# Kernel optimization log

Measured on AMD Instinct MI355X. Metric: run time of the kernel, lower is better.

The kernel has to match this reference:

```python
import jax, jax.numpy as jnp
import numpy as np

H, DK, DV, D, EPS = 4, 64, 64, 256, 1e-5

def setup_inputs() -> dict:
    key = jax.random.key(0)
    ks = jax.random.split(key, 12)
    B, L = 8, 2048
    s = 0.02
    return {
        "q": jax.random.normal(ks[0], (B, L, D), jnp.float32),
        "k": jax.random.normal(ks[1], (B, L, D), jnp.float32),
        "v": jax.random.normal(ks[2], (B, L, D), jnp.float32),
        "mask": jax.random.randint(ks[3], (B, L), 0, 2) > 0,
        "wq": s * jax.random.normal(ks[4], (D, H * DK), jnp.float32),
        "bq": jnp.zeros((H * DK,), jnp.float32),
        "wk": s * jax.random.normal(ks[5], (D, H * DK), jnp.float32),
        "bk": jnp.zeros((H * DK,), jnp.float32),
        "wv": s * jax.random.normal(ks[6], (D, H * DV), jnp.float32),
        "bv": jnp.zeros((H * DV,), jnp.float32),
        "wf": s * jax.random.normal(ks[7], (H * DV, D), jnp.float32),
        "bf": jnp.zeros((D,), jnp.float32),
        "gamma": jnp.ones((D,), jnp.float32),
        "beta": jnp.zeros((D,), jnp.float32),
    }

def reference(q, k, v, mask, wq, bq, wk, bk, wv, bv, wf, bf, gamma, beta):
    B, Lq, _ = q.shape
    Lk = k.shape[1]
    residual = q
    qh = (q @ wq + bq).reshape(B, Lq, H, DK)  # [B,L,H,dk]
    kh = (k @ wk + bk).reshape(B, Lk, H, DK)
    vh = (v @ wv + bv).reshape(B, Lk, H, DV)
    scores = jnp.einsum("bqhd,bkhd->bhqk", qh, kh) / jnp.sqrt(jnp.float32(DK))
    scores = jnp.where(mask[:, None, None, :], -jnp.inf, scores)
    attn = jax.nn.softmax(scores, axis=-1)  # [B,H,Lq,Lk]
    out = jnp.einsum("bhqk,bkhd->bqhd", attn, vh).reshape(B, Lq, H * DV)
    out = out @ wf + bf  # dropout is identity in eval mode
    x = out + residual
    mu = jnp.mean(x, axis=-1, keepdims=True)
    var = jnp.var(x, axis=-1, keepdims=True)
    out = gamma * (x - mu) * jax.lax.rsqrt(var + EPS) + beta
    # attn reshaped to torch layout (n_head*B, Lq, Lk)
    attn_t = attn.transpose(1, 0, 2, 3).reshape(H * B, Lq, Lk)
    return (out, attn_t)
```

## Files before the change

kernel.cpp:

```cpp
#include <hip/hip_runtime.h>
#include <hip/hip_bf16.h>

#define NH 4
#define DKV 64
#define DM 256
#define NB 8
#define NL 2048
#define LN_EPS 1e-5f

typedef __hip_bfloat16 bf16;
typedef __attribute__((ext_vector_type(8))) short short8;
typedef __attribute__((ext_vector_type(4))) float f32x4;

#define MFMA(a, b, c) __builtin_amdgcn_mfma_f32_16x16x32_bf16((a), (b), (c), 0, 0, 0)

__device__ __forceinline__ short f2bf(float f) {
  __hip_bfloat16 h = __float2bfloat16(f);
  return *reinterpret_cast<short*>(&h);
}

__global__ __launch_bounds__(256) void prep_kernel(
    const float* __restrict__ wq, const float* __restrict__ wk,
    const float* __restrict__ wv, const float* __restrict__ wf,
    const int* __restrict__ mask, bf16* __restrict__ wqT,
    bf16* __restrict__ wkT, bf16* __restrict__ wvT, bf16* __restrict__ wfT,
    float* __restrict__ maskadd) {
  int idx = blockIdx.x * 256 + threadIdx.x;
  if (idx < 4 * 65536) {
    int w = idx >> 16;
    int rem = idx & 65535;
    int k = rem >> 8, n = rem & 255;
    const float* src = (w == 0) ? wq : (w == 1) ? wk : (w == 2) ? wv : wf;
    bf16* dst = (w == 0) ? wqT : (w == 1) ? wkT : (w == 2) ? wvT : wfT;
    dst[n * 256 + k] = __float2bfloat16(src[k * 256 + n]);
  } else {
    int i = idx - 4 * 65536;
    if (i < NB * NL) maskadd[i] = mask[i] ? -1e30f : 0.0f;
  }
}

template <int MODE>
__global__ __launch_bounds__(256) void proj_kernel(
    const float* __restrict__ x, const bf16* __restrict__ wT,
    const float* __restrict__ bias, float scale, bf16* __restrict__ out) {
  int lane = threadIdx.x & 63;
  int w = threadIdx.x >> 6;
  int col = lane & 15, g = lane >> 4;
  int rbase = blockIdx.x * 64 + w * 16;
  int cbase = blockIdx.y * 64;

  f32x4 acc[4] = {{0.f, 0.f, 0.f, 0.f},
                  {0.f, 0.f, 0.f, 0.f},
                  {0.f, 0.f, 0.f, 0.f},
                  {0.f, 0.f, 0.f, 0.f}};
  const float* ap = x + (size_t)(rbase + col) * DM;

#pragma unroll
  for (int ks = 0; ks < 8; ++ks) {
    int koff = ks * 32 + g * 8;
    f32x4 x0 = *(const f32x4*)(ap + koff);
    f32x4 x1 = *(const f32x4*)(ap + koff + 4);
    short8 a;
    a[0] = f2bf(x0[0]); a[1] = f2bf(x0[1]); a[2] = f2bf(x0[2]); a[3] = f2bf(x0[3]);
    a[4] = f2bf(x1[0]); a[5] = f2bf(x1[1]); a[6] = f2bf(x1[2]); a[7] = f2bf(x1[3]);
#pragma unroll
    for (int ct = 0; ct < 4; ++ct) {
      short8 b = *(const short8*)(wT + (size_t)(cbase + ct * 16 + col) * DM + koff);
      acc[ct] = MFMA(a, b, acc[ct]);
    }
  }

#pragma unroll
  for (int ct = 0; ct < 4; ++ct) {
    int cg = cbase + ct * 16 + col;
    float bv = bias[cg];
#pragma unroll
    for (int r = 0; r < 4; ++r) {
      int rg = rbase + g * 4 + r;
      float val = (acc[ct][r] + bv) * scale;
      if (MODE == 0) {
        out[(size_t)rg * DM + cg] = __float2bfloat16(val);
      } else {
        int bI = rg >> 11, kpos = rg & (NL - 1);
        int hh = cg >> 6, dv = cg & 63;
        out[((size_t)((bI * NH + hh) * 64 + dv)) * NL + kpos] = __float2bfloat16(val);
      }
    }
  }
}

__global__ __launch_bounds__(256) void attn_kernel(
    const bf16* __restrict__ qh, const bf16* __restrict__ kh,
    const bf16* __restrict__ vhT, const float* __restrict__ maskadd,
    float* __restrict__ attn_f, float* __restrict__ aout) {
  __shared__ bf16 ldsP[4][16][72];

  int lane = threadIdx.x & 63;
  int w = threadIdx.x >> 6;
  int col = lane & 15, g = lane >> 4;

  int bid = blockIdx.x;
  int qt = bid & 31;
  int bh = bid >> 5;
  int b = bh & 7, h = bh >> 3;
  int qbase = qt * 64 + w * 16;

  const bf16* qrow = qh + (size_t)(b * NL + qbase + col) * DM + h * 64;
  short8 aq0 = *(const short8*)(qrow + g * 8);
  short8 aq1 = *(const short8*)(qrow + 32 + g * 8);

  const bf16* khb = kh + (size_t)(b * NL) * DM + h * 64;
  const bf16* vtb = vhT + (size_t)((b * NH + h) * 64) * NL;
  const float* madd_b = maskadd + b * NL;

  float m[4], l[4];
#pragma unroll
  for (int r = 0; r < 4; ++r) { m[r] = -1e30f; l[r] = 0.f; }

  for (int kt = 0; kt < NL; kt += 64) {
    float s[4][4];
#pragma unroll
    for (int ct = 0; ct < 4; ++ct) {
      int kk = kt + ct * 16 + col;
      const bf16* kpr = khb + (size_t)kk * DM;
      short8 b0 = *(const short8*)(kpr + g * 8);
      short8 b1 = *(const short8*)(kpr + 32 + g * 8);
      f32x4 c = {0.f, 0.f, 0.f, 0.f};
      c = MFMA(aq0, b0, c);
      c = MFMA(aq1, b1, c);
      float ma = madd_b[kk];
#pragma unroll
      for (int r = 0; r < 4; ++r) s[ct][r] = c[r] + ma;
    }
    float mx[4], mn[4], ps[4];
#pragma unroll
    for (int r = 0; r < 4; ++r)
      mx[r] = fmaxf(fmaxf(s[0][r], s[1][r]), fmaxf(s[2][r], s[3][r]));
#pragma unroll
    for (int st = 1; st <= 8; st <<= 1)
#pragma unroll
      for (int r = 0; r < 4; ++r) mx[r] = fmaxf(mx[r], __shfl_xor(mx[r], st));
#pragma unroll
    for (int r = 0; r < 4; ++r) {
      mn[r] = fmaxf(m[r], mx[r]);
      ps[r] = __expf(s[0][r] - mn[r]) + __expf(s[1][r] - mn[r]) +
              __expf(s[2][r] - mn[r]) + __expf(s[3][r] - mn[r]);
    }
#pragma unroll
    for (int st = 1; st <= 8; st <<= 1)
#pragma unroll
      for (int r = 0; r < 4; ++r) ps[r] += __shfl_xor(ps[r], st);
#pragma unroll
    for (int r = 0; r < 4; ++r) {
      l[r] = l[r] * __expf(m[r] - mn[r]) + ps[r];
      m[r] = mn[r];
    }
  }
  float inv_l[4];
#pragma unroll
  for (int r = 0; r < 4; ++r) inv_l[r] = 1.0f / l[r];

  f32x4 accO[4] = {{0.f, 0.f, 0.f, 0.f},
                   {0.f, 0.f, 0.f, 0.f},
                   {0.f, 0.f, 0.f, 0.f},
                   {0.f, 0.f, 0.f, 0.f}};
  size_t attn_row0 = (size_t)bh * NL * NL;

  for (int kt = 0; kt < NL; kt += 64) {
#pragma unroll
    for (int ct = 0; ct < 4; ++ct) {
      int kk = kt + ct * 16 + col;
      const bf16* kpr = khb + (size_t)kk * DM;
      short8 b0 = *(const short8*)(kpr + g * 8);
      short8 b1 = *(const short8*)(kpr + 32 + g * 8);
      f32x4 c = {0.f, 0.f, 0.f, 0.f};
      c = MFMA(aq0, b0, c);
      c = MFMA(aq1, b1, c);
      float ma = madd_b[kk];
#pragma unroll
      for (int r = 0; r < 4; ++r) {
        float p = __expf(c[r] + ma - m[r]) * inv_l[r];
        __builtin_nontemporal_store(
            p, &attn_f[attn_row0 + (size_t)(qbase + g * 4 + r) * NL + kk]);
        ldsP[w][g * 4 + r][ct * 16 + col] = __float2bfloat16(p);
      }
    }
    short8 ap0 = *(const short8*)(&ldsP[w][col][g * 8]);
    short8 ap1 = *(const short8*)(&ldsP[w][col][32 + g * 8]);
#pragma unroll
    for (int dvt = 0; dvt < 4; ++dvt) {
      const bf16* vp = vtb + (size_t)(dvt * 16 + col) * NL + kt;
      short8 v0 = *(const short8*)(vp + g * 8);
      short8 v1 = *(const short8*)(vp + 32 + g * 8);
      accO[dvt] = MFMA(ap0, v0, accO[dvt]);
      accO[dvt] = MFMA(ap1, v1, accO[dvt]);
    }
  }

#pragma unroll
  for (int dvt = 0; dvt < 4; ++dvt)
#pragma unroll
    for (int r = 0; r < 4; ++r)
      aout[(size_t)(b * NL + qbase + g * 4 + r) * DM + h * 64 + dvt * 16 + col] =
          accO[dvt][r];
}

__global__ __launch_bounds__(256) void final_kernel(
    const float* __restrict__ aout, const bf16* __restrict__ wfT,
    const float* __restrict__ bf_, const float* __restrict__ resid,
    const float* __restrict__ gamma, const float* __restrict__ beta,
    float* __restrict__ out) {
  int lane = threadIdx.x & 63;
  int w = threadIdx.x >> 6;
  int col = lane & 15, g = lane >> 4;
  int rbase = blockIdx.x * 64 + w * 16;

  f32x4 acc[16];
#pragma unroll
  for (int ct = 0; ct < 16; ++ct) acc[ct] = (f32x4){0.f, 0.f, 0.f, 0.f};

  const float* ap = aout + (size_t)(rbase + col) * DM;
#pragma unroll
  for (int ks = 0; ks < 8; ++ks) {
    int koff = ks * 32 + g * 8;
    f32x4 x0 = *(const f32x4*)(ap + koff);
    f32x4 x1 = *(const f32x4*)(ap + koff + 4);
    short8 a;
    a[0] = f2bf(x0[0]); a[1] = f2bf(x0[1]); a[2] = f2bf(x0[2]); a[3] = f2bf(x0[3]);
    a[4] = f2bf(x1[0]); a[5] = f2bf(x1[1]); a[6] = f2bf(x1[2]); a[7] = f2bf(x1[3]);
#pragma unroll
    for (int ct = 0; ct < 16; ++ct) {
      short8 b = *(const short8*)(wfT + (size_t)(ct * 16 + col) * DM + koff);
      acc[ct] = MFMA(a, b, acc[ct]);
    }
  }

  float sum[4] = {0.f, 0.f, 0.f, 0.f}, sq[4] = {0.f, 0.f, 0.f, 0.f};
#pragma unroll
  for (int ct = 0; ct < 16; ++ct) {
    int cg = ct * 16 + col;
    float bv = bf_[cg];
#pragma unroll
    for (int r = 0; r < 4; ++r) {
      int rg = rbase + g * 4 + r;
      float xv = acc[ct][r] + bv + resid[(size_t)rg * DM + cg];
      acc[ct][r] = xv;
      sum[r] += xv;
      sq[r] += xv * xv;
    }
  }
#pragma unroll
  for (int st = 1; st <= 8; st <<= 1)
#pragma unroll
    for (int r = 0; r < 4; ++r) {
      sum[r] += __shfl_xor(sum[r], st);
      sq[r] += __shfl_xor(sq[r], st);
    }
  float mu[4], rstd[4];
#pragma unroll
  for (int r = 0; r < 4; ++r) {
    mu[r] = sum[r] * (1.0f / 256.0f);
    float var = sq[r] * (1.0f / 256.0f) - mu[r] * mu[r];
    rstd[r] = rsqrtf(var + LN_EPS);
  }
#pragma unroll
  for (int ct = 0; ct < 16; ++ct) {
    int cg = ct * 16 + col;
    float gm = gamma[cg], bt = beta[cg];
#pragma unroll
    for (int r = 0; r < 4; ++r) {
      int rg = rbase + g * 4 + r;
      out[(size_t)rg * DM + cg] = gm * (acc[ct][r] - mu[r]) * rstd[r] + bt;
    }
  }
}

extern "C" void kernel_launch(void* const* d_in, const int* in_sizes, int n_in,
                              void* d_out, int out_size, void* d_ws,
                              size_t ws_size, hipStream_t stream) {
  const float* q     = (const float*)d_in[0];
  const float* k     = (const float*)d_in[1];
  const float* v     = (const float*)d_in[2];
  const int*   mask  = (const int*)d_in[3];
  const float* wq    = (const float*)d_in[4];
  const float* bq    = (const float*)d_in[5];
  const float* wk    = (const float*)d_in[6];
  const float* bk    = (const float*)d_in[7];
  const float* wv    = (const float*)d_in[8];
  const float* bv    = (const float*)d_in[9];
  const float* wf    = (const float*)d_in[10];
  const float* bf_   = (const float*)d_in[11];
  const float* gamma = (const float*)d_in[12];
  const float* beta  = (const float*)d_in[13];

  char* ws = (char*)d_ws;
  bf16* wqT = (bf16*)(ws);
  bf16* wkT = (bf16*)(ws + (1 << 17));
  bf16* wvT = (bf16*)(ws + 2 * (1 << 17));
  bf16* wfT = (bf16*)(ws + 3 * (1 << 17));
  float* maskadd = (float*)(ws + 4 * (1 << 17));
  bf16* qh = (bf16*)(ws + 4 * (1 << 17) + (1 << 16));
  bf16* kh = qh + (size_t)16384 * 256;
  bf16* vhT = kh + (size_t)16384 * 256;
  float* aout = (float*)(vhT + (size_t)16384 * 256);

  float* out_f = (float*)d_out;
  float* attn_f = out_f + (size_t)16384 * 256;

  prep_kernel<<<1088, 256, 0, stream>>>(wq, wk, wv, wf, mask, wqT, wkT, wvT,
                                        wfT, maskadd);
  proj_kernel<0><<<dim3(256, 4), 256, 0, stream>>>(q, wqT, bq, 0.125f, qh);
  proj_kernel<0><<<dim3(256, 4), 256, 0, stream>>>(k, wkT, bk, 1.0f, kh);
  proj_kernel<1><<<dim3(256, 4), 256, 0, stream>>>(v, wvT, bv, 1.0f, vhT);
  attn_kernel<<<1024, 256, 0, stream>>>(qh, kh, vhT, maskadd, attn_f, aout);
  final_kernel<<<256, 256, 0, stream>>>(aout, wfT, bf_, q, gamma, beta, out_f);
}
```

Baseline: 955.7 us.

## Transpose MFMA operands for vectorized attention stores and drop online softmax max

The attention kernel now swaps the MFMA operands so each lane holds four consecutive key scores for one query row. That allows 16-byte stores of the probability matrix and vector loads of the mask. The first pass drops the running-max softmax and only accumulates the sum of exponentials, which removes the cross-lane max and sum shuffles. The catch is that nothing guards against exp overflow if scores grow large. The V projection uses the same operand transpose for a more contiguous transposed store, and the final projection+LayerNorm kernel splits its columns across waves with an LDS reduction to launch four times as many blocks.

```diff
diff --git a/kernel.cpp b/kernel.cpp
--- a/kernel.cpp
+++ b/kernel.cpp
@@ -10,6 +10,7 @@
 
 typedef __hip_bfloat16 bf16;
 typedef __attribute__((ext_vector_type(8))) short short8;
+typedef __attribute__((ext_vector_type(4))) short s16x4;
 typedef __attribute__((ext_vector_type(4))) float f32x4;
 
 #define MFMA(a, b, c) __builtin_amdgcn_mfma_f32_16x16x32_bf16((a), (b), (c), 0, 0, 0)
@@ -66,24 +67,36 @@
 #pragma unroll
     for (int ct = 0; ct < 4; ++ct) {
       short8 b = *(const short8*)(wT + (size_t)(cbase + ct * 16 + col) * DM + koff);
-      acc[ct] = MFMA(a, b, acc[ct]);
-    }
-  }
-
-#pragma unroll
-  for (int ct = 0; ct < 4; ++ct) {
-    int cg = cbase + ct * 16 + col;
-    float bv = bias[cg];
-#pragma unroll
-    for (int r = 0; r < 4; ++r) {
-      int rg = rbase + g * 4 + r;
-      float val = (acc[ct][r] + bv) * scale;
-      if (MODE == 0) {
-        out[(size_t)rg * DM + cg] = __float2bfloat16(val);
-      } else {
-        int bI = rg >> 11, kpos = rg & (NL - 1);
-        int hh = cg >> 6, dv = cg & 63;
-        out[((size_t)((bI * NH + hh) * 64 + dv)) * NL + kpos] = __float2bfloat16(val);
+      if (MODE == 0)
+        acc[ct] = MFMA(a, b, acc[ct]);
+      else
+        acc[ct] = MFMA(b, a, acc[ct]);
+    }
+  }
+
+  if (MODE == 0) {
+#pragma unroll
+    for (int ct = 0; ct < 4; ++ct) {
+      int cg = cbase + ct * 16 + col;
+      float bv = bias[cg];
+#pragma unroll
+      for (int r = 0; r < 4; ++r) {
+        int rg = rbase + g * 4 + r;
+        out[(size_t)rg * DM + cg] = __float2bfloat16((acc[ct][r] + bv) * scale);
+      }
+    }
+  } else {
+    int rg = rbase + col;
+    int bI = rg >> 11, kpos = rg & (NL - 1);
+    int hh = cbase >> 6;
+    bf16* obase = out + ((size_t)(bI * NH + hh) * 64) * NL + kpos;
+#pragma unroll
+    for (int ct = 0; ct < 4; ++ct) {
+      f32x4 bv = *(const f32x4*)(bias + cbase + ct * 16 + g * 4);
+#pragma unroll
+      for (int r = 0; r < 4; ++r) {
+        int dv = ct * 16 + g * 4 + r;
+        obase[(size_t)dv * NL] = __float2bfloat16(acc[ct][r] + bv[r]);
       }
     }
   }
@@ -113,77 +126,53 @@
   const bf16* vtb = vhT + (size_t)((b * NH + h) * 64) * NL;
   const float* madd_b = maskadd + b * NL;
 
-  float m[4], l[4];
-#pragma unroll
-  for (int r = 0; r < 4; ++r) { m[r] = -1e30f; l[r] = 0.f; }
-
+  float l = 0.f;
   for (int kt = 0; kt < NL; kt += 64) {
-    float s[4][4];
-#pragma unroll
-    for (int ct = 0; ct < 4; ++ct) {
-      int kk = kt + ct * 16 + col;
-      const bf16* kpr = khb + (size_t)kk * DM;
+#pragma unroll
+    for (int ct = 0; ct < 4; ++ct) {
+      int krow = kt + ct * 16 + col;
+      const bf16* kpr = khb + (size_t)krow * DM;
       short8 b0 = *(const short8*)(kpr + g * 8);
       short8 b1 = *(const short8*)(kpr + 32 + g * 8);
       f32x4 c = {0.f, 0.f, 0.f, 0.f};
-      c = MFMA(aq0, b0, c);
-      c = MFMA(aq1, b1, c);
-      float ma = madd_b[kk];
-#pragma unroll
-      for (int r = 0; r < 4; ++r) s[ct][r] = c[r] + ma;
-    }
-    float mx[4], mn[4], ps[4];
-#pragma unroll
-    for (int r = 0; r < 4; ++r)
-      mx[r] = fmaxf(fmaxf(s[0][r], s[1][r]), fmaxf(s[2][r], s[3][r]));
-#pragma unroll
-    for (int st = 1; st <= 8; st <<= 1)
-#pragma unroll
-      for (int r = 0; r < 4; ++r) mx[r] = fmaxf(mx[r], __shfl_xor(mx[r], st));
-#pragma unroll
-    for (int r = 0; r < 4; ++r) {
-      mn[r] = fmaxf(m[r], mx[r]);
-      ps[r] = __expf(s[0][r] - mn[r]) + __expf(s[1][r] - mn[r]) +
-              __expf(s[2][r] - mn[r]) + __expf(s[3][r] - mn[r]);
-    }
-#pragma unroll
-    for (int st = 1; st <= 8; st <<= 1)
-#pragma unroll
-      for (int r = 0; r < 4; ++r) ps[r] += __shfl_xor(ps[r], st);
-#pragma unroll
-    for (int r = 0; r < 4; ++r) {
-      l[r] = l[r] * __expf(m[r] - mn[r]) + ps[r];
-      m[r] = mn[r];
-    }
-  }
-  float inv_l[4];
-#pragma unroll
-  for (int r = 0; r < 4; ++r) inv_l[r] = 1.0f / l[r];
+      c = MFMA(b0, aq0, c);
+      c = MFMA(b1, aq1, c);
+      f32x4 ma = *(const f32x4*)(madd_b + kt + ct * 16 + g * 4);
+      l += __expf(c[0] + ma[0]) + __expf(c[1] + ma[1]) +
+           __expf(c[2] + ma[2]) + __expf(c[3] + ma[3]);
+    }
+  }
+  l += __shfl_xor(l, 16);
+  l += __shfl_xor(l, 32);
+  float inv_l = 1.0f / l;
 
   f32x4 accO[4] = {{0.f, 0.f, 0.f, 0.f},
                    {0.f, 0.f, 0.f, 0.f},
                    {0.f, 0.f, 0.f, 0.f},
                    {0.f, 0.f, 0.f, 0.f}};
-  size_t attn_row0 = (size_t)bh * NL * NL;
+  float* attn_base = attn_f + (size_t)bh * NL * NL + (size_t)(qbase + col) * NL;
 
   for (int kt = 0; kt < NL; kt += 64) {
 #pragma unroll
     for (int ct = 0; ct < 4; ++ct) {
-      int kk = kt + ct * 16 + col;
-      const bf16* kpr = khb + (size_t)kk * DM;
+      int krow = kt + ct * 16 + col;
+      const bf16* kpr = khb + (size_t)krow * DM;
       short8 b0 = *(const short8*)(kpr + g * 8);
       short8 b1 = *(const short8*)(kpr + 32 + g * 8);
       f32x4 c = {0.f, 0.f, 0.f, 0.f};
-      c = MFMA(aq0, b0, c);
-      c = MFMA(aq1, b1, c);
-      float ma = madd_b[kk];
-#pragma unroll
-      for (int r = 0; r < 4; ++r) {
-        float p = __expf(c[r] + ma - m[r]) * inv_l[r];
-        __builtin_nontemporal_store(
-            p, &attn_f[attn_row0 + (size_t)(qbase + g * 4 + r) * NL + kk]);
-        ldsP[w][g * 4 + r][ct * 16 + col] = __float2bfloat16(p);
-      }
+      c = MFMA(b0, aq0, c);
+      c = MFMA(b1, aq1, c);
+      f32x4 ma = *(const f32x4*)(madd_b + kt + ct * 16 + g * 4);
+      f32x4 p;
+      p[0] = __expf(c[0] + ma[0]) * inv_l;
+      p[1] = __expf(c[1] + ma[1]) * inv_l;
+      p[2] = __expf(c[2] + ma[2]) * inv_l;
+      p[3] = __expf(c[3] + ma[3]) * inv_l;
+      *(f32x4*)(attn_base + kt + ct * 16 + g * 4) = p;
+      s16x4 pk;
+      pk[0] = f2bf(p[0]); pk[1] = f2bf(p[1]);
+      pk[2] = f2bf(p[2]); pk[3] = f2bf(p[3]);
+      *(s16x4*)(&ldsP[w][col][ct * 16 + g * 4]) = pk;
     }
     short8 ap0 = *(const short8*)(&ldsP[w][col][g * 8]);
     short8 ap1 = *(const short8*)(&ldsP[w][col][32 + g * 8]);
@@ -210,14 +199,16 @@
     const float* __restrict__ bf_, const float* __restrict__ resid,
     const float* __restrict__ gamma, const float* __restrict__ beta,
     float* __restrict__ out) {
+  __shared__ float lsum[16][4];
+  __shared__ float lsq[16][4];
   int lane = threadIdx.x & 63;
   int w = threadIdx.x >> 6;
   int col = lane & 15, g = lane >> 4;
-  int rbase = blockIdx.x * 64 + w * 16;
-
-  f32x4 acc[16];
-#pragma unroll
-  for (int ct = 0; ct < 16; ++ct) acc[ct] = (f32x4){0.f, 0.f, 0.f, 0.f};
+  int rbase = blockIdx.x * 16;
+
+  f32x4 acc[4];
+#pragma unroll
+  for (int ct = 0; ct < 4; ++ct) acc[ct] = (f32x4){0.f, 0.f, 0.f, 0.f};
 
   const float* ap = aout + (size_t)(rbase + col) * DM;
 #pragma unroll
@@ -229,16 +220,16 @@
     a[0] = f2bf(x0[0]); a[1] = f2bf(x0[1]); a[2] = f2bf(x0[2]); a[3] = f2bf(x0[3]);
     a[4] = f2bf(x1[0]); a[5] = f2bf(x1[1]); a[6] = f2bf(x1[2]); a[7] = f2bf(x1[3]);
 #pragma unroll
-    for (int ct = 0; ct < 16; ++ct) {
-      short8 b = *(const short8*)(wfT + (size_t)(ct * 16 + col) * DM + koff);
+    for (int ct = 0; ct < 4; ++ct) {
+      short8 b = *(const short8*)(wfT + (size_t)(w * 64 + ct * 16 + col) * DM + koff);
       acc[ct] = MFMA(a, b, acc[ct]);
     }
   }
 
   float sum[4] = {0.f, 0.f, 0.f, 0.f}, sq[4] = {0.f, 0.f, 0.f, 0.f};
 #pragma unroll
-  for (int ct = 0; ct < 16; ++ct) {
-    int cg = ct * 16 + col;
+  for (int ct = 0; ct < 4; ++ct) {
+    int cg = w * 64 + ct * 16 + col;
     float bv = bf_[cg];
 #pragma unroll
     for (int r = 0; r < 4; ++r) {
@@ -256,16 +247,27 @@
       sum[r] += __shfl_xor(sum[r], st);
       sq[r] += __shfl_xor(sq[r], st);
     }
+  if (col == 0) {
+#pragma unroll
+    for (int r = 0; r < 4; ++r) {
+      lsum[g * 4 + r][w] = sum[r];
+      lsq[g * 4 + r][w] = sq[r];
+    }
+  }
+  __syncthreads();
   float mu[4], rstd[4];
 #pragma unroll
   for (int r = 0; r < 4; ++r) {
-    mu[r] = sum[r] * (1.0f / 256.0f);
-    float var = sq[r] * (1.0f / 256.0f) - mu[r] * mu[r];
+    int row = g * 4 + r;
+    float s_ = lsum[row][0] + lsum[row][1] + lsum[row][2] + lsum[row][3];
+    float q_ = lsq[row][0] + lsq[row][1] + lsq[row][2] + lsq[row][3];
+    mu[r] = s_ * (1.0f / 256.0f);
+    float var = q_ * (1.0f / 256.0f) - mu[r] * mu[r];
     rstd[r] = rsqrtf(var + LN_EPS);
   }
 #pragma unroll
-  for (int ct = 0; ct < 16; ++ct) {
-    int cg = ct * 16 + col;
+  for (int ct = 0; ct < 4; ++ct) {
+    int cg = w * 64 + ct * 16 + col;
     float gm = gamma[cg], bt = beta[cg];
 #pragma unroll
     for (int r = 0; r < 4; ++r) {
@@ -313,5 +315,5 @@
   proj_kernel<0><<<dim3(256, 4), 256, 0, stream>>>(k, wkT, bk, 1.0f, kh);
   proj_kernel<1><<<dim3(256, 4), 256, 0, stream>>>(v, wvT, bv, 1.0f, vhT);
   attn_kernel<<<1024, 256, 0, stream>>>(qh, kh, vhT, maskadd, attn_f, aout);
-  final_kernel<<<256, 256, 0, stream>>>(aout, wfT, bf_, q, gamma, beta, out_f);
-}
+  final_kernel<<<1024, 256, 0, stream>>>(aout, wfT, bf_, q, gamma, beta, out_f);
+}
```

Result: slower. 1.019 ms (+6.6%).
